# Kernel optimization log

Measured on AMD Instinct MI355X. Metric: run time of the kernel, lower is better.

Reference implementation:

```python
import jax, jax.numpy as jnp
import numpy as np


def setup_inputs() -> dict:
    key = jax.random.key(0)
    k1, k2, k3, k4 = jax.random.split(key, 4)
    B, T, D, H = 4, 4096, 1024, 64
    x = jax.random.normal(k1, (B, T, D), dtype=jnp.float32)
    # nn.Linear(n_embd, head_size, bias=False): store as [D, H] so x @ W matches
    scale = 1.0 / np.sqrt(D)
    Wq = jax.random.normal(k2, (D, H), dtype=jnp.float32) * scale
    Wk = jax.random.normal(k3, (D, H), dtype=jnp.float32) * scale
    Wv = jax.random.normal(k4, (D, H), dtype=jnp.float32) * scale
    return {"x": x, "Wq": Wq, "Wk": Wk, "Wv": Wv}


def reference(x, Wq, Wk, Wv):
    B, T, D = x.shape
    q = jnp.einsum('btd,dh->bth', x, Wq)
    k = jnp.einsum('btd,dh->bth', x, Wk)
    v = jnp.einsum('btd,dh->bth', x, Wv)
    # NOTE: original scales by D**-0.5 where D = n_embd (input dim), not head_size
    scores = jnp.einsum('bth,bsh->bts', q, k) * (D ** -0.5)  # [B,T,T]
    causal = jnp.tril(jnp.ones((T, T), dtype=bool))
    scores = jnp.where(causal, scores, -jnp.inf)
    attn = jax.nn.softmax(scores, axis=-1)
    return jnp.einsum('bts,bsh->bth', attn, v)
```

## Files before the change

kernel.cpp:

```cpp
#include <hip/hip_runtime.h>
#include <hip/hip_bf16.h>
#include <math.h>

typedef __attribute__((ext_vector_type(8))) short bf16x8;
typedef __attribute__((ext_vector_type(4))) float f32x4;
typedef __attribute__((ext_vector_type(16))) float f32x16;
typedef __attribute__((ext_vector_type(2))) unsigned uint2v;

#define MFMA16(A, B, C) __builtin_amdgcn_mfma_f32_16x16x32_bf16(A, B, C, 0, 0, 0)
#define MFMA32(A, B, C) __builtin_amdgcn_mfma_f32_32x32x16_bf16(A, B, C, 0, 0, 0)
#define LOG2E 1.44269504f
#define MB 5.7707801f

__device__ __forceinline__ short f2bf(float f) {
  union { __hip_bfloat16 b; short s; } v;
  v.b = __float2bfloat16(f);
  return v.s;
}

__device__ __forceinline__ float bf2f(short s) {
  union { unsigned u; float f; } v;
  v.u = ((unsigned)(unsigned short)s) << 16;
  return v.f;
}

__device__ __forceinline__ bf16x8 cvt8(float4 a, float4 b) {
  bf16x8 r;
  r[0] = f2bf(a.x); r[1] = f2bf(a.y); r[2] = f2bf(a.z); r[3] = f2bf(a.w);
  r[4] = f2bf(b.x); r[5] = f2bf(b.y); r[6] = f2bf(b.z); r[7] = f2bf(b.w);
  return r;
}

__device__ __forceinline__ unsigned cvt_pk(float lo, float hi) {
  unsigned r;
  asm("v_cvt_pk_bf16_f32 %0, %1, %2" : "=v"(r) : "v"(lo), "v"(hi));
  return r;
}

__device__ __forceinline__ void glds16(const void* g, void* l) {
  __builtin_amdgcn_global_load_lds(
      (const __attribute__((address_space(1))) unsigned int*)g,
      (__attribute__((address_space(3))) unsigned int*)l, 16, 0, 0);
}

__device__ __forceinline__ float xhalf_sum(float x) {
  uint2v r = __builtin_amdgcn_permlane32_swap(__float_as_uint(x), __float_as_uint(x),
                                              false, false);
  return __uint_as_float(r[0]) + __uint_as_float(r[1]);
}

__global__ __launch_bounds__(256) void prep_w(const float* __restrict__ Wq,
                                              const float* __restrict__ Wk,
                                              const float* __restrict__ Wv,
                                              short* __restrict__ Wt) {
  __shared__ float ls[64][65];
  const int wsel = blockIdx.x >> 4;
  const int dt = blockIdx.x & 15;
  const float* W = (wsel == 0) ? Wq : ((wsel == 1) ? Wk : Wv);
  const float scale = (wsel == 0) ? (0.03125f * LOG2E) : 1.0f;
  const int d0 = dt * 64;
  const int rr = threadIdx.x >> 4;
  const int cc = threadIdx.x & 15;
#pragma unroll
  for (int p = 0; p < 4; ++p) {
    int d = rr + p * 16;
    float4 v = *(const float4*)(W + (size_t)(d0 + d) * 64 + cc * 4);
    ls[d][cc * 4 + 0] = v.x; ls[d][cc * 4 + 1] = v.y;
    ls[d][cc * 4 + 2] = v.z; ls[d][cc * 4 + 3] = v.w;
  }
  __syncthreads();
#pragma unroll
  for (int p = 0; p < 4; ++p) {
    int h = rr + p * 16;
    short4 o;
    o.x = f2bf(ls[cc * 4 + 0][h] * scale);
    o.y = f2bf(ls[cc * 4 + 1][h] * scale);
    o.z = f2bf(ls[cc * 4 + 2][h] * scale);
    o.w = f2bf(ls[cc * 4 + 3][h] * scale);
    *(short4*)(Wt + (size_t)(wsel * 64 + h) * 1024 + d0 + cc * 4) = o;
  }
}

__global__ __launch_bounds__(512, 4) void qkv_kernel(const float* __restrict__ x,
                                                     const short* __restrict__ Wt,
                                                     short* __restrict__ qo,
                                                     short* __restrict__ ko,
                                                     short* __restrict__ vT) {
  __shared__ __align__(16) char pool[81920];
  const int tid = threadIdx.x;
  const int wave = tid >> 6, lane = tid & 63;
  const int lr = lane & 15, lq = lane >> 4;
  const int wm = wave & 1, wn = wave >> 1;
  const int m0 = blockIdx.x * 64;

  f32x4 acc[2][3];
#pragma unroll
  for (int mi = 0; mi < 2; ++mi)
#pragma unroll
    for (int j = 0; j < 3; ++j) acc[mi][j] = f32x4{0.f, 0.f, 0.f, 0.f};

  const int xrow0 = wave * 4 + (lane >> 4);
  const int col16 = lane & 15;
  const float* xg[2];
#pragma unroll
  for (int r = 0; r < 2; ++r) {
    int srow = xrow0 + r * 32;
    xg[r] = x + (size_t)(m0 + srow) * 1024 + ((col16 ^ (srow & 7)) << 2);
  }
  const int wrow0 = wave * 8 + (lane >> 3);
  const int col8 = lane & 7;
  const short* wg[3];
#pragma unroll
  for (int r = 0; r < 3; ++r) {
    int n = wrow0 + r * 64;
    wg[r] = Wt + (size_t)n * 1024 + ((col8 ^ (n & 7)) << 3);
  }
  const int dst_off = wave * 1024;

#define STAGEQ(c, t)                                                        \
  {                                                                         \
    char* xb_ = pool + (c) * 40960;                                         \
    _Pragma("unroll") for (int r = 0; r < 2; ++r)                           \
        glds16(xg[r] + (t) * 64, xb_ + r * 8192 + dst_off);                 \
    _Pragma("unroll") for (int r = 0; r < 3; ++r)                           \
        glds16(wg[r] + (t) * 64, xb_ + 16384 + r * 8192 + dst_off);         \
  }

  STAGEQ(0, 0)
  __syncthreads();

  int cur = 0;
  for (int t = 0; t < 16; ++t) {
    if (t < 15) STAGEQ(cur ^ 1, t + 1)
    const char* xb = pool + cur * 40960;
    const char* wb = xb + 16384;
#pragma unroll
    for (int kc = 0; kc < 2; ++kc) {
      bf16x8 bfg[3];
#pragma unroll
      for (int j = 0; j < 3; ++j) {
        int n = (wn * 3 + j) * 16 + lr;
        int unit = kc * 4 + lq;
        bfg[j] = *(const bf16x8*)(wb + n * 128 + ((unit ^ (n & 7)) << 4));
      }
#pragma unroll
      for (int mi = 0; mi < 2; ++mi) {
        int row = wm * 32 + mi * 16 + lr;
        int p = kc * 4 + lq;
        const char* xr = xb + row * 256;
        float4 a0 = *(const float4*)(xr + (((2 * p) ^ (row & 7)) << 4));
        float4 a1 = *(const float4*)(xr + (((2 * p + 1) ^ (row & 7)) << 4));
        bf16x8 af = cvt8(a0, a1);
#pragma unroll
        for (int j = 0; j < 3; ++j) acc[mi][j] = MFMA16(af, bfg[j], acc[mi][j]);
      }
    }
    __syncthreads();
    cur ^= 1;
  }
#undef STAGEQ

  short* els = (short*)pool;
#pragma unroll
  for (int j = 0; j < 3; ++j) {
    int nt = wn * 3 + j;
#pragma unroll
    for (int mi = 0; mi < 2; ++mi) {
      if (nt < 8) {
#pragma unroll
        for (int r = 0; r < 4; ++r) {
          int mloc = wm * 32 + mi * 16 + lq * 4 + r;
          els[mloc * 136 + nt * 16 + lr] = f2bf(acc[mi][j][r]);
        }
      } else {
        int m = m0 + wm * 32 + mi * 16 + lq * 4;
        short4 h;
        h.x = f2bf(acc[mi][j][0]); h.y = f2bf(acc[mi][j][1]);
        h.z = f2bf(acc[mi][j][2]); h.w = f2bf(acc[mi][j][3]);
        *(short4*)(vT + ((m >> 12) << 18) + ((nt * 16 + lr - 128) << 12) +
                   (m & 4095)) = h;
      }
    }
  }
  __syncthreads();
  {
    const int m = tid >> 3, nq = tid & 7;
    bf16x8 vq = *(const bf16x8*)(els + m * 136 + nq * 8);
    bf16x8 vk = *(const bf16x8*)(els + m * 136 + 64 + nq * 8);
    *(bf16x8*)(qo + (size_t)(m0 + m) * 64 + nq * 8) = vq;
    *(bf16x8*)(ko + (size_t)(m0 + m) * 64 + nq * 8) = vk;
  }
}

__global__ __launch_bounds__(256) void attn_partial(const short* __restrict__ qbuf,
                                                    const short* __restrict__ kbuf,
                                                    const short* __restrict__ vbuf,
                                                    short* __restrict__ Op,
                                                    float* __restrict__ lp) {
  __shared__ __align__(16) char kv_lds[2][16384];
  const int id = blockIdx.x;
  const int b = id & 3;
  const int u = id >> 2;
  int k = 0;
  while (u >= 2 * (k + 1) * (k + 2)) ++k;
  const int t = u - 2 * k * (k + 1);
  const int qtl = t / (k + 1);
  const int seg = t - qtl * (k + 1);
  const int qt = k * 4 + qtl;
  const int kv_lo = seg << 9;
  const int kv_hi = (seg == k) ? (qt * 128 + 128) : ((seg + 1) << 9);

  const int tid = threadIdx.x;
  const int wv = tid >> 6, lane = tid & 63;
  const int l31 = lane & 31, hi = lane >> 5;
  const int qr0 = qt * 128 + wv * 32;
  const int qglob = qr0 + l31;

  const short* qb = qbuf + ((size_t)b << 18);
  const short* kb = kbuf + ((size_t)b << 18);
  const short* vb = vbuf + ((size_t)b << 18);

  bf16x8 bq[4];
#pragma unroll
  for (int c = 0; c < 4; ++c)
    bq[c] = *(const bf16x8*)(qb + (size_t)(qr0 + l31) * 64 + c * 16 + hi * 8);

  const int sr = (wv << 4) + (lane >> 3);
  const int swz_s = ((lane & 7) ^ (lane >> 3)) << 3;
  const short* ksrc = kb + (size_t)sr * 64 + swz_s;
  const short* vsrc = vb + (size_t)sr * 4096 + swz_s;
  const int kdst = (wv * 2) * 1024;
  const int vdst = 8192 + (wv * 2) * 1024;

#define STAGE(c, KV0)                                                       \
  {                                                                         \
    char* base_ = kv_lds[c];                                                \
    glds16(ksrc + (size_t)(KV0) * 64, base_ + kdst);                        \
    glds16(ksrc + (size_t)((KV0) + 8) * 64, base_ + kdst + 1024);           \
    glds16(vsrc + (KV0), base_ + vdst);                                     \
    glds16(vsrc + 8 * 4096 + (KV0), base_ + vdst + 1024);                   \
  }

  f32x16 o0, o1;
#pragma unroll
  for (int r = 0; r < 16; ++r) { o0[r] = 0.f; o1[r] = 0.f; }
  float lrow = 0.f;

  union U8 { unsigned u[4]; bf16x8 v; };
  const int swz_r = (l31 & 7);

  STAGE(0, kv_lo)
  __syncthreads();

  int cur = 0;
  for (int kv0 = kv_lo; kv0 < kv_hi; kv0 += 64) {
    if (kv0 + 64 < kv_hi) STAGE(cur ^ 1, kv0 + 64)

    if (kv0 <= qr0 + 31) {
      const int kv1 = kv0 + 32;
      const char* kl = kv_lds[cur];
      const char* vl = kv_lds[cur] + 8192;
      bf16x8 ka[4], kc[4], va[8];
#pragma unroll
      for (int c = 0; c < 4; ++c) {
        ka[c] = *(const bf16x8*)(kl + l31 * 128 + (((c * 2 + hi) ^ swz_r) << 4));
        kc[c] = *(const bf16x8*)(kl + (32 + l31) * 128 + (((c * 2 + hi) ^ swz_r) << 4));
      }
#pragma unroll
      for (int h = 0; h < 2; ++h)
#pragma unroll
        for (int p = 0; p < 4; ++p)
          va[h * 4 + p] = *(const bf16x8*)(vl + (32 * h + l31) * 128 +
                                           (((2 * p + hi) ^ swz_r) << 4));

      f32x16 s0, s1;
#pragma unroll
      for (int r = 0; r < 16; ++r) { s0[r] = 0.f; s1[r] = 0.f; }
#pragma unroll
      for (int c = 0; c < 4; ++c) {
        s0 = MFMA32(ka[c], bq[c], s0);
        s1 = MFMA32(kc[c], bq[c], s1);
      }

      if (kv0 + 31 > qr0) {
#pragma unroll
        for (int r = 0; r < 16; ++r)
          if (kv0 + (r & 3) + 8 * (r >> 2) + 4 * hi > qglob) s0[r] = -1e30f;
      }
      if (kv1 + 31 > qr0) {
#pragma unroll
        for (int r = 0; r < 16; ++r)
          if (kv1 + (r & 3) + 8 * (r >> 2) + 4 * hi > qglob) s1[r] = -1e30f;
      }

      float p0[16], p1[16];
#pragma unroll
      for (int r = 0; r < 16; ++r) {
        p0[r] = exp2f(s0[r] - MB);
        p1[r] = exp2f(s1[r] - MB);
      }
      float a8[8];
#pragma unroll
      for (int r = 0; r < 8; ++r) a8[r] = (p0[r] + p0[r + 8]) + (p1[r] + p1[r + 8]);
      float s4 = ((a8[0] + a8[4]) + (a8[1] + a8[5])) +
                 ((a8[2] + a8[6]) + (a8[3] + a8[7]));
      lrow += xhalf_sum(s4);

#define MAKE_FRAGS(P, UA, UB)                                                  \
      {                                                                        \
        unsigned c0 = cvt_pk(P[0], P[1]), c1 = cvt_pk(P[2], P[3]);             \
        unsigned c2 = cvt_pk(P[4], P[5]), c3 = cvt_pk(P[6], P[7]);             \
        unsigned c4 = cvt_pk(P[8], P[9]), c5 = cvt_pk(P[10], P[11]);           \
        unsigned c6 = cvt_pk(P[12], P[13]), c7 = cvt_pk(P[14], P[15]);         \
        uint2v rA = __builtin_amdgcn_permlane32_swap(c0, c2, false, false);    \
        uint2v rB = __builtin_amdgcn_permlane32_swap(c1, c3, false, false);    \
        uint2v rC = __builtin_amdgcn_permlane32_swap(c4, c6, false, false);    \
        uint2v rD = __builtin_amdgcn_permlane32_swap(c5, c7, false, false);    \
        UA.u[0] = rA[0]; UA.u[2] = rA[1];                                      \
        UA.u[1] = rB[0]; UA.u[3] = rB[1];                                      \
        UB.u[0] = rC[0]; UB.u[2] = rC[1];                                      \
        UB.u[1] = rD[0]; UB.u[3] = rD[1];                                      \
      }
      U8 pa00, pa01, pa10, pa11;
      MAKE_FRAGS(p0, pa00, pa01)
      MAKE_FRAGS(p1, pa10, pa11)
#undef MAKE_FRAGS

      o0 = MFMA32(va[0], pa00.v, o0);
      o0 = MFMA32(va[1], pa01.v, o0);
      o0 = MFMA32(va[2], pa10.v, o0);
      o0 = MFMA32(va[3], pa11.v, o0);
      o1 = MFMA32(va[4], pa00.v, o1);
      o1 = MFMA32(va[5], pa01.v, o1);
      o1 = MFMA32(va[6], pa10.v, o1);
      o1 = MFMA32(va[7], pa11.v, o1);
    }

    __syncthreads();
    cur ^= 1;
  }
#undef STAGE

  const int pid = b * 144 + u;
  short* Ob = Op + (size_t)pid * 8192;
#pragma unroll
  for (int r = 0; r < 16; ++r) {
    int hd = (r & 3) + 8 * (r >> 2) + 4 * hi;
    Ob[hd * 128 + wv * 32 + l31] = f2bf(o0[r]);
    Ob[(32 + hd) * 128 + wv * 32 + l31] = f2bf(o1[r]);
  }
  if (hi == 0) lp[pid * 128 + wv * 32 + l31] = lrow;
}

__global__ __launch_bounds__(256) void attn_combine(const short* __restrict__ Op,
                                                    const float* __restrict__ lp,
                                                    float* __restrict__ out) {
  __shared__ float ls[32][128];
  const int qt = blockIdx.x;
  const int b = blockIdx.y;
  const int zh = blockIdx.z;
  const int k = qt >> 2;
  const int nseg = k + 1;
  const int base = b * 144 + 2 * k * (k + 1) + (qt - 4 * k) * (k + 1);

  const int qc = threadIdx.x & 127, hh = threadIdx.x >> 7;
  float lsum = 0.f;
  for (int s = 0; s < nseg; ++s) lsum += lp[(base + s) * 128 + qc];
  const float inv = 1.0f / lsum;

  float osum[16];
#pragma unroll
  for (int i = 0; i < 16; ++i) osum[i] = 0.f;
  for (int s = 0; s < nseg; ++s) {
    const short* Ob = Op + (size_t)(base + s) * 8192;
#pragma unroll
    for (int i = 0; i < 16; ++i)
      osum[i] += bf2f(Ob[(zh * 32 + hh * 16 + i) * 128 + qc]);
  }
#pragma unroll
  for (int i = 0; i < 16; ++i) ls[hh * 16 + i][qc] = osum[i] * inv;
  __syncthreads();

  const int row = threadIdx.x >> 1, ch = (threadIdx.x & 1) * 16;
  float4 w4[4];
#pragma unroll
  for (int g4 = 0; g4 < 4; ++g4) {
    w4[g4].x = ls[ch + g4 * 4 + 0][row];
    w4[g4].y = ls[ch + g4 * 4 + 1][row];
    w4[g4].z = ls[ch + g4 * 4 + 2][row];
    w4[g4].w = ls[ch + g4 * 4 + 3][row];
  }
  float* op = out + ((size_t)b * 4096 + (size_t)qt * 128 + row) * 64 + zh * 32 + ch;
#pragma unroll
  for (int g4 = 0; g4 < 4; ++g4) *(float4*)(op + g4 * 4) = w4[g4];
}

extern "C" void kernel_launch(void* const* d_in, const int* in_sizes, int n_in,
                              void* d_out, int out_size, void* d_ws, size_t ws_size,
                              hipStream_t stream) {
  const float* x = (const float*)d_in[0];
  const float* Wq = (const float*)d_in[1];
  const float* Wk = (const float*)d_in[2];
  const float* Wv = (const float*)d_in[3];
  float* out = (float*)d_out;

  char* w = (char*)d_ws;
  short* qb = (short*)(w);
  short* kb = (short*)(w + (size_t)2 * 1024 * 1024);
  short* vT = (short*)(w + (size_t)4 * 1024 * 1024);
  short* Wt = (short*)(w + (size_t)6 * 1024 * 1024);
  float* lp = (float*)(w + (size_t)7040 * 1024);
  short* Op = (short*)(w + (size_t)7424 * 1024);

  prep_w<<<48, 256, 0, stream>>>(Wq, Wk, Wv, Wt);
  qkv_kernel<<<256, 512, 0, stream>>>(x, Wt, qb, kb, vT);
  attn_partial<<<576, 256, 0, stream>>>(qb, kb, vT, Op, lp);
  attn_combine<<<dim3(32, 4, 2), 256, 0, stream>>>(Op, lp, out);
}
```

Before: 69.62 us.

## Halve QKV tile height and split attention KV into 256-wide segments

The QKV projection now uses 32-row tiles with 256-thread blocks. Each wave covers three 16-column output tiles over the full 192 columns, so twice as many blocks launch with less shared memory each. The attention split-KV partitioning changes from 512-wide to 256-wide segments, which grows the partial grid from 576 to 1088 blocks. The combine indexing and workspace offsets are updated to match. The goal is better load balance and occupancy on the GPU. The cost is that each W tile is reloaded by more QKV blocks, and there are more partial outputs to write and reduce.

```diff
diff --git a/kernel.cpp b/kernel.cpp
--- a/kernel.cpp
+++ b/kernel.cpp
@@ -81,17 +81,16 @@
   }
 }
 
-__global__ __launch_bounds__(512, 4) void qkv_kernel(const float* __restrict__ x,
+__global__ __launch_bounds__(256, 2) void qkv_kernel(const float* __restrict__ x,
                                                      const short* __restrict__ Wt,
                                                      short* __restrict__ qo,
                                                      short* __restrict__ ko,
                                                      short* __restrict__ vT) {
-  __shared__ __align__(16) char pool[81920];
+  __shared__ __align__(16) char pool[65536];
   const int tid = threadIdx.x;
   const int wave = tid >> 6, lane = tid & 63;
   const int lr = lane & 15, lq = lane >> 4;
-  const int wm = wave & 1, wn = wave >> 1;
-  const int m0 = blockIdx.x * 64;
+  const int m0 = blockIdx.x * 32;
 
   f32x4 acc[2][3];
 #pragma unroll
@@ -104,26 +103,26 @@
   const float* xg[2];
 #pragma unroll
   for (int r = 0; r < 2; ++r) {
-    int srow = xrow0 + r * 32;
-    xg[r] = x + (size_t)(m0 + srow) * 1024 + ((col16 ^ (srow & 7)) << 2);
-  }
-  const int wrow0 = wave * 8 + (lane >> 3);
-  const int col8 = lane & 7;
-  const short* wg[3];
-#pragma unroll
-  for (int r = 0; r < 3; ++r) {
-    int n = wrow0 + r * 64;
-    wg[r] = Wt + (size_t)n * 1024 + ((col8 ^ (n & 7)) << 3);
-  }
-  const int dst_off = wave * 1024;
+    int row = xrow0 + r * 16;
+    xg[r] = x + (size_t)(m0 + row) * 1024 + ((col16 ^ (row & 7)) << 2);
+  }
+  const int wswz = ((lane & 7) ^ (lane >> 3)) << 3;
+  const short* wg[6];
+#pragma unroll
+  for (int r = 0; r < 6; ++r) {
+    int n = wave * 8 + (lane >> 3) + r * 32;
+    wg[r] = Wt + (size_t)n * 1024 + wswz;
+  }
+  const int xdst = wave * 1024;
+  const int wdst = 8192 + wave * 1024;
 
 #define STAGEQ(c, t)                                                        \
   {                                                                         \
-    char* xb_ = pool + (c) * 40960;                                         \
-    _Pragma("unroll") for (int r = 0; r < 2; ++r)                           \
-        glds16(xg[r] + (t) * 64, xb_ + r * 8192 + dst_off);                 \
-    _Pragma("unroll") for (int r = 0; r < 3; ++r)                           \
-        glds16(wg[r] + (t) * 64, xb_ + 16384 + r * 8192 + dst_off);         \
+    char* pb = pool + (c) * 32768;                                          \
+    glds16(xg[0] + (t) * 64, pb + xdst);                                    \
+    glds16(xg[1] + (t) * 64, pb + xdst + 4096);                             \
+    _Pragma("unroll") for (int r = 0; r < 6; ++r)                           \
+        glds16(wg[r] + (t) * 64, pb + wdst + r * 4096);                     \
   }
 
   STAGEQ(0, 0)
@@ -132,20 +131,20 @@
   int cur = 0;
   for (int t = 0; t < 16; ++t) {
     if (t < 15) STAGEQ(cur ^ 1, t + 1)
-    const char* xb = pool + cur * 40960;
-    const char* wb = xb + 16384;
+    const char* xb = pool + cur * 32768;
+    const char* wb = xb + 8192;
 #pragma unroll
     for (int kc = 0; kc < 2; ++kc) {
       bf16x8 bfg[3];
 #pragma unroll
       for (int j = 0; j < 3; ++j) {
-        int n = (wn * 3 + j) * 16 + lr;
+        int n = (wave * 3 + j) * 16 + lr;
         int unit = kc * 4 + lq;
         bfg[j] = *(const bf16x8*)(wb + n * 128 + ((unit ^ (n & 7)) << 4));
       }
 #pragma unroll
       for (int mi = 0; mi < 2; ++mi) {
-        int row = wm * 32 + mi * 16 + lr;
+        int row = mi * 16 + lr;
         int p = kc * 4 + lq;
         const char* xr = xb + row * 256;
         float4 a0 = *(const float4*)(xr + (((2 * p) ^ (row & 7)) << 4));
@@ -163,17 +162,17 @@
   short* els = (short*)pool;
 #pragma unroll
   for (int j = 0; j < 3; ++j) {
-    int nt = wn * 3 + j;
+    int nt = wave * 3 + j;
 #pragma unroll
     for (int mi = 0; mi < 2; ++mi) {
       if (nt < 8) {
 #pragma unroll
         for (int r = 0; r < 4; ++r) {
-          int mloc = wm * 32 + mi * 16 + lq * 4 + r;
+          int mloc = mi * 16 + lq * 4 + r;
           els[mloc * 136 + nt * 16 + lr] = f2bf(acc[mi][j][r]);
         }
       } else {
-        int m = m0 + wm * 32 + mi * 16 + lq * 4;
+        int m = m0 + mi * 16 + lq * 4;
         short4 h;
         h.x = f2bf(acc[mi][j][0]); h.y = f2bf(acc[mi][j][1]);
         h.z = f2bf(acc[mi][j][2]); h.w = f2bf(acc[mi][j][3]);
@@ -201,14 +200,11 @@
   const int id = blockIdx.x;
   const int b = id & 3;
   const int u = id >> 2;
-  int k = 0;
-  while (u >= 2 * (k + 1) * (k + 2)) ++k;
-  const int t = u - 2 * k * (k + 1);
-  const int qtl = t / (k + 1);
-  const int seg = t - qtl * (k + 1);
-  const int qt = k * 4 + qtl;
-  const int kv_lo = seg << 9;
-  const int kv_hi = (seg == k) ? (qt * 128 + 128) : ((seg + 1) << 9);
+  int qt = 0, base = 0;
+  while (u >= base + (qt >> 1) + 1) { base += (qt >> 1) + 1; ++qt; }
+  const int seg = u - base;
+  const int kv_lo = seg << 8;
+  const int kv_hi = (seg == (qt >> 1)) ? (qt * 128 + 128) : ((seg + 1) << 8);
 
   const int tid = threadIdx.x;
   const int wv = tid >> 6, lane = tid & 63;
@@ -341,7 +337,7 @@
   }
 #undef STAGE
 
-  const int pid = b * 144 + u;
+  const int pid = b * 272 + u;
   short* Ob = Op + (size_t)pid * 8192;
 #pragma unroll
   for (int r = 0; r < 16; ++r) {
@@ -359,9 +355,9 @@
   const int qt = blockIdx.x;
   const int b = blockIdx.y;
   const int zh = blockIdx.z;
-  const int k = qt >> 2;
-  const int nseg = k + 1;
-  const int base = b * 144 + 2 * k * (k + 1) + (qt - 4 * k) * (k + 1);
+  const int m = qt >> 1, e = qt & 1;
+  const int nseg = m + 1;
+  const int base = b * 272 + qt + m * (m - 1) + e * m;
 
   const int qc = threadIdx.x & 127, hh = threadIdx.x >> 7;
   float lsum = 0.f;
@@ -409,11 +405,11 @@
   short* kb = (short*)(w + (size_t)2 * 1024 * 1024);
   short* vT = (short*)(w + (size_t)4 * 1024 * 1024);
   short* Wt = (short*)(w + (size_t)6 * 1024 * 1024);
-  float* lp = (float*)(w + (size_t)7040 * 1024);
+  float* lp = (float*)(w + (size_t)6656 * 1024);
   short* Op = (short*)(w + (size_t)7424 * 1024);
 
   prep_w<<<48, 256, 0, stream>>>(Wq, Wk, Wv, Wt);
-  qkv_kernel<<<256, 512, 0, stream>>>(x, Wt, qb, kb, vT);
-  attn_partial<<<576, 256, 0, stream>>>(qb, kb, vT, Op, lp);
+  qkv_kernel<<<512, 256, 0, stream>>>(x, Wt, qb, kb, vT);
+  attn_partial<<<1088, 256, 0, stream>>>(qb, kb, vT, Op, lp);
   attn_combine<<<dim3(32, 4, 2), 256, 0, stream>>>(Op, lp, out);
 }
```

After: 68.66 us (median of 2 runs). About the same (-1.4%).

## Triple-buffer QKV projection loads and split attention KV into smaller segments

Applied to the files above, without the earlier changes.

The QKV projection kernel moves from double to triple buffering in shared memory (120KB), using explicit vmcnt waits and raw barriers so two tiles are in flight while one is computed. The attention partial kernel now splits the causal KV range into 256-wide segments instead of 512-wide, roughly doubling the grid (1088 blocks) for better load balance and occupancy across CUs. The combine kernel's indexing and the workspace layout for the partial l-sums are updated to match. The tradeoffs are more partial outputs for the combine step to read, and larger LDS use that limits QKV blocks per CU.

```diff
diff --git a/kernel.cpp b/kernel.cpp
--- a/kernel.cpp
+++ b/kernel.cpp
@@ -86,7 +86,7 @@
                                                      short* __restrict__ qo,
                                                      short* __restrict__ ko,
                                                      short* __restrict__ vT) {
-  __shared__ __align__(16) char pool[81920];
+  __shared__ __align__(16) char pool[122880];
   const int tid = threadIdx.x;
   const int wave = tid >> 6, lane = tid & 63;
   const int lr = lane & 15, lq = lane >> 4;
@@ -126,40 +126,54 @@
         glds16(wg[r] + (t) * 64, xb_ + 16384 + r * 8192 + dst_off);         \
   }
 
+#define QCOMP(XB)                                                           \
+  {                                                                         \
+    const char* xb = (XB);                                                  \
+    const char* wb = xb + 16384;                                            \
+    _Pragma("unroll") for (int kc = 0; kc < 2; ++kc) {                      \
+      bf16x8 bfg[3];                                                        \
+      _Pragma("unroll") for (int j = 0; j < 3; ++j) {                       \
+        int n = (wn * 3 + j) * 16 + lr;                                     \
+        int unit = kc * 4 + lq;                                             \
+        bfg[j] = *(const bf16x8*)(wb + n * 128 + ((unit ^ (n & 7)) << 4));  \
+      }                                                                     \
+      _Pragma("unroll") for (int mi = 0; mi < 2; ++mi) {                    \
+        int row = wm * 32 + mi * 16 + lr;                                   \
+        int p = kc * 4 + lq;                                                \
+        const char* xr = xb + row * 256;                                    \
+        float4 a0 = *(const float4*)(xr + (((2 * p) ^ (row & 7)) << 4));    \
+        float4 a1 = *(const float4*)(xr + (((2 * p + 1) ^ (row & 7)) << 4));\
+        bf16x8 af = cvt8(a0, a1);                                           \
+        _Pragma("unroll") for (int j = 0; j < 3; ++j)                       \
+            acc[mi][j] = MFMA16(af, bfg[j], acc[mi][j]);                    \
+      }                                                                     \
+    }                                                                       \
+  }
+
   STAGEQ(0, 0)
+  STAGEQ(1, 1)
+
+  int bt = 2, bc = 0;
+  for (int t = 0; t < 14; ++t) {
+    STAGEQ(bt, t + 2)
+    asm volatile("s_waitcnt vmcnt(10)" ::: "memory");
+    __builtin_amdgcn_s_barrier();
+    QCOMP(pool + bc * 40960)
+    __builtin_amdgcn_s_barrier();
+    bt = (bt == 2) ? 0 : bt + 1;
+    bc = (bc == 2) ? 0 : bc + 1;
+  }
+  asm volatile("s_waitcnt vmcnt(5)" ::: "memory");
+  __builtin_amdgcn_s_barrier();
+  QCOMP(pool + 2 * 40960)
+  __builtin_amdgcn_s_barrier();
+  asm volatile("s_waitcnt vmcnt(0)" ::: "memory");
+  __builtin_amdgcn_s_barrier();
+  QCOMP(pool + 0 * 40960)
+#undef STAGEQ
+#undef QCOMP
+
   __syncthreads();
-
-  int cur = 0;
-  for (int t = 0; t < 16; ++t) {
-    if (t < 15) STAGEQ(cur ^ 1, t + 1)
-    const char* xb = pool + cur * 40960;
-    const char* wb = xb + 16384;
-#pragma unroll
-    for (int kc = 0; kc < 2; ++kc) {
-      bf16x8 bfg[3];
-#pragma unroll
-      for (int j = 0; j < 3; ++j) {
-        int n = (wn * 3 + j) * 16 + lr;
-        int unit = kc * 4 + lq;
-        bfg[j] = *(const bf16x8*)(wb + n * 128 + ((unit ^ (n & 7)) << 4));
-      }
-#pragma unroll
-      for (int mi = 0; mi < 2; ++mi) {
-        int row = wm * 32 + mi * 16 + lr;
-        int p = kc * 4 + lq;
-        const char* xr = xb + row * 256;
-        float4 a0 = *(const float4*)(xr + (((2 * p) ^ (row & 7)) << 4));
-        float4 a1 = *(const float4*)(xr + (((2 * p + 1) ^ (row & 7)) << 4));
-        bf16x8 af = cvt8(a0, a1);
-#pragma unroll
-        for (int j = 0; j < 3; ++j) acc[mi][j] = MFMA16(af, bfg[j], acc[mi][j]);
-      }
-    }
-    __syncthreads();
-    cur ^= 1;
-  }
-#undef STAGEQ
-
   short* els = (short*)pool;
 #pragma unroll
   for (int j = 0; j < 3; ++j) {
@@ -201,14 +215,11 @@
   const int id = blockIdx.x;
   const int b = id & 3;
   const int u = id >> 2;
-  int k = 0;
-  while (u >= 2 * (k + 1) * (k + 2)) ++k;
-  const int t = u - 2 * k * (k + 1);
-  const int qtl = t / (k + 1);
-  const int seg = t - qtl * (k + 1);
-  const int qt = k * 4 + qtl;
-  const int kv_lo = seg << 9;
-  const int kv_hi = (seg == k) ? (qt * 128 + 128) : ((seg + 1) << 9);
+  int qt = 0, base = 0;
+  while (u >= base + (qt >> 1) + 1) { base += (qt >> 1) + 1; ++qt; }
+  const int seg = u - base;
+  const int kv_lo = seg << 8;
+  const int kv_hi = (seg == (qt >> 1)) ? (qt * 128 + 128) : ((seg + 1) << 8);
 
   const int tid = threadIdx.x;
   const int wv = tid >> 6, lane = tid & 63;
@@ -341,7 +352,7 @@
   }
 #undef STAGE
 
-  const int pid = b * 144 + u;
+  const int pid = b * 272 + u;
   short* Ob = Op + (size_t)pid * 8192;
 #pragma unroll
   for (int r = 0; r < 16; ++r) {
@@ -359,9 +370,9 @@
   const int qt = blockIdx.x;
   const int b = blockIdx.y;
   const int zh = blockIdx.z;
-  const int k = qt >> 2;
-  const int nseg = k + 1;
-  const int base = b * 144 + 2 * k * (k + 1) + (qt - 4 * k) * (k + 1);
+  const int m = qt >> 1, e = qt & 1;
+  const int nseg = m + 1;
+  const int base = b * 272 + qt + m * (m - 1) + e * m;
 
   const int qc = threadIdx.x & 127, hh = threadIdx.x >> 7;
   float lsum = 0.f;
@@ -409,11 +420,11 @@
   short* kb = (short*)(w + (size_t)2 * 1024 * 1024);
   short* vT = (short*)(w + (size_t)4 * 1024 * 1024);
   short* Wt = (short*)(w + (size_t)6 * 1024 * 1024);
-  float* lp = (float*)(w + (size_t)7040 * 1024);
+  float* lp = (float*)(w + (size_t)6656 * 1024);
   short* Op = (short*)(w + (size_t)7424 * 1024);
 
   prep_w<<<48, 256, 0, stream>>>(Wq, Wk, Wv, Wt);
   qkv_kernel<<<256, 512, 0, stream>>>(x, Wt, qb, kb, vT);
-  attn_partial<<<576, 256, 0, stream>>>(qb, kb, vT, Op, lp);
+  attn_partial<<<1088, 256, 0, stream>>>(qb, kb, vT, Op, lp);
   attn_combine<<<dim3(32, 4, 2), 256, 0, stream>>>(Op, lp, out);
 }
```

Result: no change. 70.58 us (+1.4%).
